# Kernel optimization log

Measured on AMD Instinct MI355X. Metric: run time of the kernel, lower is better.

The kernel has to match this reference:

```python
import jax, jax.numpy as jnp
import numpy as np

H = 64; DS = 32; DT = 24; ED = 16; OUT = 2
N = 10000       # nodes per type
E = 40000       # edges per edge type (before self loops)
MAX_DEG = 12    # static padded neighbor-sequence length (PyG to_dense_batch max); excess dropped


def setup_inputs() -> dict:
    key = jax.random.key(0)
    k = iter(jax.random.split(key, 40))
    def lin(o, i):
        s = 1.0 / np.sqrt(i)
        return jax.random.uniform(next(k), (o, i), jnp.float32, -s, s)
    inp = {}
    inp["x_source"] = jax.random.normal(next(k), (N, DS), jnp.float32)
    inp["x_target"] = jax.random.normal(next(k), (N, DT), jnp.float32)
    # 4 edge types in order [src->src, tgt->tgt, src->tgt, tgt->src], each [2, E]
    inp["edges"] = jax.random.randint(next(k), (4, 2, E), 0, N, dtype=jnp.int32)
    inp["edge_attr_st"] = jax.random.normal(next(k), (E, ED), jnp.float32)
    # node encoders (Linear-ReLU-Dropout(eval)-Linear)
    inp["We_s1"] = lin(H, DS); inp["be_s1"] = jnp.zeros((H,), jnp.float32)
    inp["We_s2"] = lin(H, H);  inp["be_s2"] = jnp.zeros((H,), jnp.float32)
    inp["We_t1"] = lin(H, DT); inp["be_t1"] = jnp.zeros((H,), jnp.float32)
    inp["We_t2"] = lin(H, H);  inp["be_t2"] = jnp.zeros((H,), jnp.float32)
    # 12 SAGEConv(aggr='lstm') blocks: 3 layers x 4 edge types, stacked on dim 0
    s = 1.0 / np.sqrt(H)
    inp["Wih"] = jax.random.uniform(next(k), (12, 4 * H, H), jnp.float32, -s, s)
    inp["Whh"] = jax.random.uniform(next(k), (12, 4 * H, H), jnp.float32, -s, s)
    inp["bih"] = jax.random.uniform(next(k), (12, 4 * H), jnp.float32, -s, s)
    inp["bhh"] = jax.random.uniform(next(k), (12, 4 * H), jnp.float32, -s, s)
    inp["Wl"]  = jax.random.uniform(next(k), (12, H, H), jnp.float32, -s, s)
    inp["bl"]  = jnp.zeros((12, H), jnp.float32)
    inp["Wr"]  = jax.random.uniform(next(k), (12, H, H), jnp.float32, -s, s)
    # edge gate + edge MLP head
    inp["Wg1"] = lin(H, 2 * H);   inp["bg1"] = jnp.zeros((H,), jnp.float32)
    inp["Wg2"] = lin(1, H);       inp["bg2"] = jnp.zeros((1,), jnp.float32)
    inp["Wm1"] = lin(H, H + ED);  inp["bm1"] = jnp.zeros((H,), jnp.float32)
    inp["Wm2"] = lin(H // 2, H);  inp["bm2"] = jnp.zeros((H // 2,), jnp.float32)
    inp["Wm3"] = lin(OUT, H // 2); inp["bm3"] = jnp.zeros((OUT,), jnp.float32)
    return inp


def _lstm_last(dense, Wih, Whh, bih, bhh):
    # dense: [n, T, H] padded neighbor sequences; PyG LSTMAggregation returns lstm(x)[0][:, -1]
    n = dense.shape[0]
    h0 = jnp.zeros((n, H), dense.dtype)
    def step(carry, x_t):
        h, c = carry
        g = x_t @ Wih.T + bih + h @ Whh.T + bhh  # torch gate order: i, f, g, o
        i, f, gg, o = jnp.split(g, 4, axis=-1)
        c = jax.nn.sigmoid(f) * c + jax.nn.sigmoid(i) * jnp.tanh(gg)
        h = jax.nn.sigmoid(o) * jnp.tanh(c)
        return (h, c), None
    (h, _), _ = jax.lax.scan(step, (h0, h0), jnp.swapaxes(dense, 0, 1))
    return h


def _sage_lstm(x_src, x_dst, src, dst, Wih, Whh, bih, bhh, Wl, bl, Wr):
    n_src, n_dst = x_src.shape[0], x_dst.shape[0]
    # add_self_loops(num_nodes=n_dst): appends (i, i) for every destination node, zero edge_attr
    loop = jnp.arange(n_dst, dtype=src.dtype)
    src = jnp.concatenate([src, loop]); dst = jnp.concatenate([dst, loop])
    # sort_edge_index(sort_by_row=False): stable lexicographic (dst, src) order
    order = jnp.argsort(dst.astype(jnp.int64) * n_src + src.astype(jnp.int64))
    src_s, dst_s = src[order], dst[order]
    xj = x_src[src_s]                                   # gather neighbor feats [E', H]
    deg = jnp.zeros((n_dst,), jnp.int32).at[dst_s].add(1)
    start = jnp.cumsum(deg) - deg                       # CSR row starts
    pos = jnp.arange(dst_s.shape[0], dtype=jnp.int32) - start[dst_s]
    dense = jnp.zeros((n_dst, MAX_DEG, x_src.shape[1]), x_src.dtype)
    dense = dense.at[dst_s, pos].set(xj, mode="drop")   # pad-to-dense, drop beyond MAX_DEG
    agg = _lstm_last(dense, Wih, Whh, bih, bhh)
    # SAGEConv: lin_l(aggr) + lin_r(x_root); lin_r has no bias
    return agg @ Wl.T + bl + x_dst @ Wr.T


def reference(x_source, x_target, edges, edge_attr_st,
              We_s1, be_s1, We_s2, be_s2, We_t1, be_t1, We_t2, be_t2,
              Wih, Whh, bih, bhh, Wl, bl, Wr,
              Wg1, bg1, Wg2, bg2, Wm1, bm1, Wm2, bm2, Wm3, bm3):
    relu = jax.nn.relu
    xs = relu(x_source @ We_s1.T + be_s1) @ We_s2.T + be_s2
    xt = relu(x_target @ We_t1.T + be_t1) @ We_t2.T + be_t2

    def layer(xs, xt, L):
        specs = [(xs, xs, 0), (xt, xt, 1), (xs, xt, 2), (xt, xs, 3)]
        outs = []
        for x_src, x_dst, et in specs:
            i = L * 4 + et
            outs.append(_sage_lstm(x_src, x_dst, edges[et, 0], edges[et, 1],
                                   Wih[i], Whh[i], bih[i], bhh[i], Wl[i], bl[i], Wr[i]))
        # HeteroConv(aggr='mean'): each node type receives from exactly 2 edge types
        return 0.5 * (outs[0] + outs[3]), 0.5 * (outs[1] + outs[2])

    s1, t1 = layer(xs, xt, 0); s1, t1 = relu(s1), relu(t1)
    s2, t2 = layer(s1, t1, 1); s2, t2 = relu(s2 + s1), relu(t2 + t1)
    s3, t3 = layer(s2, t2, 2); s3, t3 = relu(s3 + s2), relu(t3 + t2)

    # edge head on the main ('source','to','target') edges (original edges, no self loops)
    se, te = s3[edges[2, 0]], t3[edges[2, 1]]
    g = jax.nn.sigmoid(relu(jnp.concatenate([se, te], -1) @ Wg1.T + bg1) @ Wg2.T + bg2)
    er = g * se + (1.0 - g) * te
    h = relu(jnp.concatenate([er, edge_attr_st], -1) @ Wm1.T + bm1)
    h = relu(h @ Wm2.T + bm2)
    return h @ Wm3.T + bm3  # [E, OUT] edge logits
```

## Files before the change

### kernel.cpp

```cpp
#include <hip/hip_runtime.h>

#define N_NODES 10000
#define N_EDGES 40000
#define HD 64
#define MAXD 12
#define CAP 32
#define YROW ((size_t)(N_NODES + 1) * 256)

typedef __attribute__((ext_vector_type(8))) short short8;
typedef __attribute__((ext_vector_type(4))) float floatx4;

#define MFMA16(A, B, C) __builtin_amdgcn_mfma_f32_16x16x32_bf16(A, B, C, 0, 0, 0)

__device__ __forceinline__ float sigmoidf_(float x) {
  return 1.0f / (1.0f + __expf(-x));
}
__device__ __forceinline__ float fma4(float4 w, float4 x, float a) {
  a = fmaf(w.x, x.x, a);
  a = fmaf(w.y, x.y, a);
  a = fmaf(w.z, x.z, a);
  return fmaf(w.w, x.w, a);
}

__device__ __forceinline__ void split_frag(float4 a, float4 b, short8& hi, short8& lo) {
  float f[8] = {a.x, a.y, a.z, a.w, b.x, b.y, b.z, b.w};
  union { short8 v; unsigned d[4]; } H, L;
#pragma unroll
  for (int p = 0; p < 4; ++p) {
    unsigned u0 = __float_as_uint(f[2 * p]);
    unsigned u1 = __float_as_uint(f[2 * p + 1]);
    H.d[p] = (u0 >> 16) | (u1 & 0xFFFF0000u);
    float l0 = f[2 * p] - __uint_as_float(u0 & 0xFFFF0000u);
    float l1 = f[2 * p + 1] - __uint_as_float(u1 & 0xFFFF0000u);
    L.d[p] = (__float_as_uint(l0) >> 16) | (__float_as_uint(l1) & 0xFFFF0000u);
  }
  hi = H.v;
  lo = L.v;
}


__global__ void scatter_kernel(const int* __restrict__ edges, int* __restrict__ cnt,
                               int* __restrict__ pool) {
  int idx = blockIdx.x * 256 + threadIdx.x;
  if (idx >= 4 * N_EDGES) return;
  int et = idx / N_EDGES, e = idx - et * N_EDGES;
  int src = edges[(et * 2) * N_EDGES + e];
  int dst = edges[(et * 2 + 1) * N_EDGES + e];
  int slot = atomicAdd(&cnt[et * N_NODES + dst], 1);
  if (slot < CAP) pool[(et * N_NODES + dst) * CAP + slot] = src;
}

__global__ void sortrows_kernel(const int* __restrict__ cnt, const int* __restrict__ pool,
                                int* __restrict__ nbr) {
  __shared__ int buf[64][CAP + 1];
  int idx = blockIdx.x * 64 + threadIdx.x;
  if (idx >= 4 * N_NODES) return;
  int n = idx % N_NODES;
  int c = cnt[idx];
  if (c > CAP) c = CAP;
  int* a = buf[threadIdx.x];
  const int* row = pool + idx * CAP;
  for (int j = 0; j < c; ++j) a[j] = row[j] * 2;
  a[c] = n * 2 + 1;
  ++c;
  for (int i2 = 1; i2 < c; ++i2) {
    int key = a[i2];
    int b = i2 - 1;
    while (b >= 0 && a[b] > key) { a[b + 1] = a[b]; --b; }
    a[b + 1] = key;
  }
  int* onbr = nbr + idx * MAXD;
  for (int t = 0; t < MAXD; ++t) onbr[t] = (t < c) ? (a[t] >> 1) : N_NODES;
}

__global__ void zero_dummy_kernel(float* __restrict__ ybase) {
  int tid = threadIdx.x;
#pragma unroll
  for (int et = 0; et < 4; ++et)
    ybase[(size_t)et * YROW + (size_t)N_NODES * 256 + tid] = 0.0f;
}


__global__ __launch_bounds__(256) void prep_wfrag_kernel(const float* __restrict__ W,
                                                         short* __restrict__ w16) {
  int gid = blockIdx.x * 256 + threadIdx.x;
  if (gid >= 384 * 64) return;
  int lane = gid & 63;
  int combo = gid >> 6;
  int kc = combo & 1;
  int g = (combo >> 1) & 3;
  int w = (combo >> 3) & 3;
  int i = combo >> 5;
  int gate = g * 64 + w * 16 + (lane & 15);
  int k0 = kc * 32 + (lane >> 4) * 8;
  const float* src = W + ((size_t)i * 256 + gate) * 64 + k0;
  float4 a = ((const float4*)src)[0];
  float4 b = ((const float4*)src)[1];
  short8 hi, lo;
  split_frag(a, b, hi, lo);
  short8* dst = (short8*)w16;
  dst[(combo * 2 + 0) * 64 + lane] = hi;
  dst[(combo * 2 + 1) * 64 + lane] = lo;
}


__global__ __launch_bounds__(256) void prep_cw_kernel(const float* __restrict__ Wl,
    const float* __restrict__ Wr, short* __restrict__ cw) {
  int gid = blockIdx.x * 256 + threadIdx.x;
  if (gid >= 144 * 64) return;
  int lane = gid & 63;
  int rest = gid >> 6;
  int combo = rest & 7;
  int mat = (rest >> 3) % 3;
  int pair = rest / 24;
  int L = pair >> 1, side = pair & 1;
  int iA = L * 4 + (side ? 1 : 0);
  int iB = L * 4 + (side ? 2 : 3);
  int wp = combo >> 1, kc = combo & 1;
  int row = wp * 16 + (lane & 15);
  int k0 = kc * 32 + (lane >> 4) * 8;
  float4 a, b;
  if (mat == 0) {
    const float* s = Wl + ((size_t)iA * 64 + row) * 64 + k0;
    a = ((const float4*)s)[0]; b = ((const float4*)s)[1];
  } else if (mat == 1) {
    const float* s = Wl + ((size_t)iB * 64 + row) * 64 + k0;
    a = ((const float4*)s)[0]; b = ((const float4*)s)[1];
  } else {
    const float* sA = Wr + ((size_t)iA * 64 + row) * 64 + k0;
    const float* sB = Wr + ((size_t)iB * 64 + row) * 64 + k0;
    float4 a1 = ((const float4*)sA)[0], b1 = ((const float4*)sA)[1];
    float4 a2 = ((const float4*)sB)[0], b2 = ((const float4*)sB)[1];
    a.x = a1.x + a2.x; a.y = a1.y + a2.y; a.z = a1.z + a2.z; a.w = a1.w + a2.w;
    b.x = b1.x + b2.x; b.y = b1.y + b2.y; b.z = b1.z + b2.z; b.w = b1.w + b2.w;
  }
  short8 hi, lo;
  split_frag(a, b, hi, lo);
  short8* dst = (short8*)cw;
  int base = ((pair * 3 + mat) * 8 + combo) * 2;
  dst[(base + 0) * 64 + lane] = hi;
  dst[(base + 1) * 64 + lane] = lo;
}


template <int IN>
__global__ __launch_bounds__(256) void encode_kernel(const float* __restrict__ x,
    const float* __restrict__ W1, const float* __restrict__ b1,
    const float* __restrict__ W2, const float* __restrict__ b2, float* __restrict__ out) {
  __shared__ float xs[4][IN];
  __shared__ float h1[4][HD];
  int w = threadIdx.x >> 6, l = threadIdx.x & 63;
  int n = blockIdx.x * 4 + w;
  if (l < IN) xs[w][l] = x[n * IN + l];
  __syncthreads();
  float acc = b1[l];
#pragma unroll
  for (int k = 0; k < IN; ++k) acc = fmaf(xs[w][k], W1[l * IN + k], acc);
  h1[w][l] = fmaxf(acc, 0.0f);
  __syncthreads();
  float acc2 = b2[l];
#pragma unroll
  for (int k = 0; k < HD; ++k) acc2 = fmaf(h1[w][k], W2[l * HD + k], acc2);
  out[n * HD + l] = acc2;
}


__global__ __launch_bounds__(256) void ygemm_mfma_kernel(const float* __restrict__ xs0,
    const float* __restrict__ xt0, const short* __restrict__ wih16L, float* __restrict__ ybase) {
  __shared__ __align__(16) float xS[16][68];
  __shared__ __align__(16) float pS[16][260];
  int et = blockIdx.y;
  const float* x = (et == 0 || et == 2) ? xs0 : xt0;
  const short8* wf = (const short8*)(wih16L + (size_t)et * 32768);
  float* y = ybase + (size_t)et * YROW;
  int tid = threadIdx.x, w = tid >> 6, l = tid & 63;
  int quad = l >> 4, n = l & 15;
  int n0 = blockIdx.x * 16;
  {
    int node = tid >> 4, f4 = tid & 15;
    float4 v = *(const float4*)(x + (size_t)(n0 + node) * 64 + f4 * 4);
    *(float4*)&xS[node][f4 * 4] = v;
  }
  short8 Bh[4][2], Bl[4][2];
#pragma unroll
  for (int wp = 0; wp < 4; ++wp)
#pragma unroll
    for (int kc = 0; kc < 2; ++kc) {
      int combo = (wp * 4 + w) * 2 + kc;
      Bh[wp][kc] = wf[(combo * 2 + 0) * 64 + l];
      Bl[wp][kc] = wf[(combo * 2 + 1) * 64 + l];
    }
  __syncthreads();
  short8 Ah[2], Al[2];
  {
    const float* hp = &xS[n][quad * 8];
    float4 q0 = *(const float4*)hp, q1 = *(const float4*)(hp + 4);
    float4 q2 = *(const float4*)(hp + 32), q3 = *(const float4*)(hp + 36);
    split_frag(q0, q1, Ah[0], Al[0]);
    split_frag(q2, q3, Ah[1], Al[1]);
  }
  floatx4 acc[4];
#pragma unroll
  for (int wp = 0; wp < 4; ++wp) {
    floatx4 a = {0.f, 0.f, 0.f, 0.f};
    a = MFMA16(Ah[0], Bh[wp][0], a);
    a = MFMA16(Ah[1], Bh[wp][1], a);
    a = MFMA16(Al[0], Bh[wp][0], a);
    a = MFMA16(Al[1], Bh[wp][1], a);
    a = MFMA16(Ah[0], Bl[wp][0], a);
    a = MFMA16(Ah[1], Bl[wp][1], a);
    acc[wp] = a;
  }
#pragma unroll
  for (int wp = 0; wp < 4; ++wp)
#pragma unroll
    for (int r = 0; r < 4; ++r)
      pS[quad * 4 + r][(wp * 16 + n) * 4 + w] = acc[wp][r];
  __syncthreads();
#pragma unroll
  for (int cc = 0; cc < 4; ++cc) {
    int g4 = cc * 256 + tid;
    int node = g4 >> 6, col = g4 & 63;
    float4 v = *(const float4*)&pS[node][col * 4];
    ((float4*)(y + (size_t)(n0 + node) * 256))[col] = v;
  }
}


__global__ __launch_bounds__(256) void lstm_mfma_kernel(const int* __restrict__ nbrAll,
    const float* __restrict__ ybase, const short* __restrict__ whh16L,
    const float* __restrict__ bihL, const float* __restrict__ bhhL, float* __restrict__ aggBase) {
  __shared__ __align__(16) unsigned pkS[2][16 * 68];
  __shared__ int nbS[16][MAXD];
  int et = blockIdx.y;
  const int* nbr = nbrAll + (size_t)et * N_NODES * MAXD;
  const float4* y4 = (const float4*)(ybase + (size_t)et * YROW);
  const short* whh16 = whh16L + (size_t)et * 32768;
  const float* bih = bihL + et * 256;
  const float* bhh = bhhL + et * 256;
  float* agg = aggBase + (size_t)et * N_NODES * HD;
  int tid = threadIdx.x, w = tid >> 6, l = tid & 63;
  int quad = l >> 4, n = l & 15, u = w * 16 + n;
  int n0 = blockIdx.x * 16;
  if (tid < 16 * MAXD) ((int*)nbS)[tid] = nbr[n0 * MAXD + tid];
  short8 Bh[4][2], Bl[4][2];
  {
    const short8* wf = (const short8*)whh16;
#pragma unroll
    for (int g = 0; g < 4; ++g)
#pragma unroll
      for (int kc = 0; kc < 2; ++kc) {
        int combo = (w * 4 + g) * 2 + kc;
        Bh[g][kc] = wf[(combo * 2 + 0) * 64 + l];
        Bl[g][kc] = wf[(combo * 2 + 1) * 64 + l];
      }
  }
  float bs[4];
#pragma unroll
  for (int g = 0; g < 4; ++g) bs[g] = bih[g * 64 + u] + bhh[g * 64 + u];
  float c[4] = {0.f, 0.f, 0.f, 0.f}, h[4];
  short8 Ah[2], Al[2];
#pragma unroll
  for (int kc = 0; kc < 2; ++kc) { Ah[kc] = (short8)0; Al[kc] = (short8)0; }
  __syncthreads();
  float4 Y[4];
#pragma unroll
  for (int r = 0; r < 4; ++r) Y[r] = y4[(size_t)nbS[quad * 4 + r][0] * 64 + u];
  for (int t = 0; t < MAXD; ++t) {
    float yg[4][4];
#pragma unroll
    for (int r = 0; r < 4; ++r) {
      yg[0][r] = Y[r].x; yg[1][r] = Y[r].y; yg[2][r] = Y[r].z; yg[3][r] = Y[r].w;
    }
    floatx4 acc[4];
#pragma unroll
    for (int g = 0; g < 4; ++g) {
      floatx4 a = {yg[g][0], yg[g][1], yg[g][2], yg[g][3]};
      a = MFMA16(Ah[0], Bh[g][0], a);
      a = MFMA16(Ah[1], Bh[g][1], a);
      a = MFMA16(Al[0], Bh[g][0], a);
      a = MFMA16(Al[1], Bh[g][1], a);
      a = MFMA16(Ah[0], Bl[g][0], a);
      a = MFMA16(Ah[1], Bl[g][1], a);
      acc[g] = a;
    }
    if (t + 1 < MAXD) {
#pragma unroll
      for (int r = 0; r < 4; ++r) Y[r] = y4[(size_t)nbS[quad * 4 + r][t + 1] * 64 + u];
    }
    int buf = (t + 1) & 1;
#pragma unroll
    for (int r = 0; r < 4; ++r) {
      float gi = acc[0][r] + bs[0];
      float gf = acc[1][r] + bs[1];
      float gg = acc[2][r] + bs[2];
      float go = acc[3][r] + bs[3];
      float a_ = __expf(-gi);
      float b_ = __expf(fminf(-(gg + gg), 60.f));
      float f_ = __expf(-gf);
      float o_ = __expf(-go);
      float p1 = 1.f + a_, p2 = 1.f + b_, p3 = 1.f + f_;
      float d1 = p1 * p2;
      float num = fmaf(c[r], d1, (1.f - b_) * p3);
      c[r] = num * __builtin_amdgcn_rcpf(p3 * d1);
      float e_ = __expf(-(c[r] + c[r]));
      h[r] = (1.f - e_) * __builtin_amdgcn_rcpf((1.f + e_) * (1.f + o_));
      unsigned ub = __float_as_uint(h[r]);
      float lo = h[r] - __uint_as_float(ub & 0xFFFF0000u);
      pkS[buf][(quad * 4 + r) * 68 + u] =
          __builtin_amdgcn_perm(ub, __float_as_uint(lo), 0x07060302u);
    }
    __syncthreads();
    if (t + 1 < MAXD) {
#pragma unroll
      for (int kc = 0; kc < 2; ++kc) {
        const unsigned* pb = &pkS[buf][n * 68 + kc * 32 + quad * 8];
        uint4 qa = *(const uint4*)pb;
        uint4 qb = *(const uint4*)(pb + 4);
        union { short8 s; unsigned d[4]; } H, L;
        H.d[0] = __builtin_amdgcn_perm(qa.y, qa.x, 0x07060302u);
        H.d[1] = __builtin_amdgcn_perm(qa.w, qa.z, 0x07060302u);
        H.d[2] = __builtin_amdgcn_perm(qb.y, qb.x, 0x07060302u);
        H.d[3] = __builtin_amdgcn_perm(qb.w, qb.z, 0x07060302u);
        L.d[0] = __builtin_amdgcn_perm(qa.y, qa.x, 0x05040100u);
        L.d[1] = __builtin_amdgcn_perm(qa.w, qa.z, 0x05040100u);
        L.d[2] = __builtin_amdgcn_perm(qb.y, qb.x, 0x05040100u);
        L.d[3] = __builtin_amdgcn_perm(qb.w, qb.z, 0x05040100u);
        Ah[kc] = H.s;
        Al[kc] = L.s;
      }
    }
  }
#pragma unroll
  for (int r = 0; r < 4; ++r)
    agg[(size_t)(n0 + quad * 4 + r) * HD + u] = h[r];
}


__global__ __launch_bounds__(256) void combine_mfma_kernel(const float* __restrict__ aggBase,
    const short* __restrict__ cwL, const float* __restrict__ blL,
    const float* __restrict__ xS0, const float* __restrict__ xT0, int has_res,
    float* __restrict__ outS, float* __restrict__ outT) {
  __shared__ __align__(16) float tS[3][16][68];
  int side = blockIdx.y;
  int etA = side ? 1 : 0, etB = side ? 2 : 3;
  const float* srcs[3];
  srcs[0] = aggBase + (size_t)etA * N_NODES * HD;
  srcs[1] = aggBase + (size_t)etB * N_NODES * HD;
  srcs[2] = side ? xT0 : xS0;
  float* out = side ? outT : outS;
  const short8* wf = (const short8*)cwL + (size_t)side * 3072;
  const float* blA = blL + etA * 64;
  const float* blB = blL + etB * 64;
  int tid = threadIdx.x, w = tid >> 6, l = tid & 63;
  int quad = l >> 4, n = l & 15;
  int n0 = blockIdx.x * 16;
  {
    int node = tid >> 4, f4 = tid & 15;
#pragma unroll
    for (int m = 0; m < 3; ++m) {
      float4 v = *(const float4*)(srcs[m] + (size_t)(n0 + node) * 64 + f4 * 4);
      *(float4*)&tS[m][node][f4 * 4] = v;
    }
  }
  short8 Bh[3][2], Bl[3][2];
#pragma unroll
  for (int m = 0; m < 3; ++m)
#pragma unroll
    for (int kc = 0; kc < 2; ++kc) {
      int base = (m * 8 + w * 2 + kc) * 2;
      Bh[m][kc] = wf[(base + 0) * 64 + l];
      Bl[m][kc] = wf[(base + 1) * 64 + l];
    }
  float bsum = blA[w * 16 + n] + blB[w * 16 + n];
  __syncthreads();
  floatx4 a = {0.f, 0.f, 0.f, 0.f};
#pragma unroll
  for (int m = 0; m < 3; ++m) {
    short8 Ah[2], Al[2];
    const float* hp = &tS[m][n][quad * 8];
    float4 q0 = *(const float4*)hp, q1 = *(const float4*)(hp + 4);
    float4 q2 = *(const float4*)(hp + 32), q3 = *(const float4*)(hp + 36);
    split_frag(q0, q1, Ah[0], Al[0]);
    split_frag(q2, q3, Ah[1], Al[1]);
    a = MFMA16(Ah[0], Bh[m][0], a);
    a = MFMA16(Ah[1], Bh[m][1], a);
    a = MFMA16(Al[0], Bh[m][0], a);
    a = MFMA16(Al[1], Bh[m][1], a);
    a = MFMA16(Ah[0], Bl[m][0], a);
    a = MFMA16(Ah[1], Bl[m][1], a);
  }
#pragma unroll
  for (int r = 0; r < 4; ++r) {
    int node = quad * 4 + r;
    float v = 0.5f * (a[r] + bsum);
    if (has_res) v += tS[2][node][w * 16 + n];
    out[(size_t)(n0 + node) * 64 + w * 16 + n] = fmaxf(v, 0.f);
  }
}


__global__ __launch_bounds__(256) void edge_head_kernel(
    const int* __restrict__ esrc, const int* __restrict__ edst, const float* __restrict__ ea,
    const float* __restrict__ s3, const float* __restrict__ t3,
    const float* __restrict__ Wg1, const float* __restrict__ bg1,
    const float* __restrict__ Wg2, const float* __restrict__ bg2,
    const float* __restrict__ Wm1, const float* __restrict__ bm1,
    const float* __restrict__ Wm2, const float* __restrict__ bm2,
    const float* __restrict__ Wm3, const float* __restrict__ bm3,
    float* __restrict__ out) {
  __shared__ __align__(16) float4 xS[64][32];
  __shared__ __align__(16) float4 eaS[64][4];
  int tid = threadIdx.x, w = tid >> 6, l = tid & 63;
  int e0 = blockIdx.x * 64;
  for (int idx = tid; idx < 2048; idx += 256) {
    int e = idx >> 5, kk = idx & 31;
    float4 v;
    if (kk < 16) v = ((const float4*)(s3 + (size_t)esrc[e0 + e] * 64))[kk];
    else         v = ((const float4*)(t3 + (size_t)edst[e0 + e] * 64))[kk - 16];
    xS[e][kk] = v;
  }
  {
    int e = tid >> 2, kk = tid & 3;
    eaS[e][kk] = ((const float4*)(ea + (size_t)(e0 + e) * 16))[kk];
  }
  __syncthreads();
  {
    float4 wr[32];
    const float4* W4 = (const float4*)(Wg1 + l * 128);
#pragma unroll
    for (int kk = 0; kk < 32; ++kk) wr[kk] = W4[kk];
    float bg = bg1[l], w2 = Wg2[l], b2 = bg2[0];
    for (int m0 = 0; m0 < 16; m0 += 4) {
      int e = w * 16 + m0;
      float a0 = bg, a1 = bg, a2 = bg, a3 = bg;
#pragma unroll
      for (int kk = 0; kk < 32; ++kk) {
        float4 wv = wr[kk];
        a0 = fma4(wv, xS[e + 0][kk], a0);
        a1 = fma4(wv, xS[e + 1][kk], a1);
        a2 = fma4(wv, xS[e + 2][kk], a2);
        a3 = fma4(wv, xS[e + 3][kk], a3);
      }
      a0 = fmaxf(a0, 0.f) * w2; a1 = fmaxf(a1, 0.f) * w2;
      a2 = fmaxf(a2, 0.f) * w2; a3 = fmaxf(a3, 0.f) * w2;
#pragma unroll
      for (int off = 32; off; off >>= 1) {
        a0 += __shfl_xor(a0, off); a1 += __shfl_xor(a1, off);
        a2 += __shfl_xor(a2, off); a3 += __shfl_xor(a3, off);
      }
      float g0 = sigmoidf_(a0 + b2), g1 = sigmoidf_(a1 + b2);
      float g2 = sigmoidf_(a2 + b2), g3 = sigmoidf_(a3 + b2);
      float* r0 = (float*)xS[e + 0]; float* r1 = (float*)xS[e + 1];
      float* r2 = (float*)xS[e + 2]; float* r3 = (float*)xS[e + 3];
      r0[l] = fmaf(g0, r0[l] - r0[64 + l], r0[64 + l]);
      r1[l] = fmaf(g1, r1[l] - r1[64 + l], r1[64 + l]);
      r2[l] = fmaf(g2, r2[l] - r2[64 + l], r2[64 + l]);
      r3[l] = fmaf(g3, r3[l] - r3[64 + l], r3[64 + l]);
    }
  }
  __syncthreads();
  {
    float4 wr[20];
    const float4* W4 = (const float4*)(Wm1 + l * 80);
#pragma unroll
    for (int kk = 0; kk < 20; ++kk) wr[kk] = W4[kk];
    float bm = bm1[l];
    float h2v[16];
    for (int m0 = 0; m0 < 16; m0 += 4) {
      int e = w * 16 + m0;
      float a0 = bm, a1 = bm, a2 = bm, a3 = bm;
#pragma unroll
      for (int kk = 0; kk < 16; ++kk) {
        float4 wv = wr[kk];
        a0 = fma4(wv, xS[e + 0][kk], a0);
        a1 = fma4(wv, xS[e + 1][kk], a1);
        a2 = fma4(wv, xS[e + 2][kk], a2);
        a3 = fma4(wv, xS[e + 3][kk], a3);
      }
#pragma unroll
      for (int kk = 0; kk < 4; ++kk) {
        float4 wv = wr[16 + kk];
        a0 = fma4(wv, eaS[e + 0][kk], a0);
        a1 = fma4(wv, eaS[e + 1][kk], a1);
        a2 = fma4(wv, eaS[e + 2][kk], a2);
        a3 = fma4(wv, eaS[e + 3][kk], a3);
      }
      h2v[m0 + 0] = fmaxf(a0, 0.f); h2v[m0 + 1] = fmaxf(a1, 0.f);
      h2v[m0 + 2] = fmaxf(a2, 0.f); h2v[m0 + 3] = fmaxf(a3, 0.f);
    }
#pragma unroll
    for (int m = 0; m < 16; ++m) ((float*)xS[w * 16 + m])[64 + l] = h2v[m];
  }
  __syncthreads();
  {
    int half = l >> 5, j = l & 31;
    float4 wr[16];
    const float4* W4 = (const float4*)(Wm2 + j * 64);
#pragma unroll
    for (int kk = 0; kk < 16; ++kk) wr[kk] = W4[kk];
    float bm = bm2[j], w3a = Wm3[j], w3b = Wm3[32 + j];
    float b3a = bm3[0], b3b = bm3[1];
    for (int mg = 0; mg < 16; mg += 2) {
      int m = mg + half, e = w * 16 + m;
      float acc = bm;
#pragma unroll
      for (int kk = 0; kk < 16; ++kk) acc = fma4(wr[kk], xS[e][16 + kk], acc);
      float h3 = fmaxf(acc, 0.f);
      float p0 = h3 * w3a, p1 = h3 * w3b;
#pragma unroll
      for (int off = 16; off; off >>= 1) {
        p0 += __shfl_xor(p0, off);
        p1 += __shfl_xor(p1, off);
      }
      if (j == 0) {
        int ge = e0 + e;
        out[ge * 2 + 0] = p0 + b3a;
        out[ge * 2 + 1] = p1 + b3b;
      }
    }
  }
}


extern "C" void kernel_launch(void* const* d_in, const int* in_sizes, int n_in, void* d_out,
                              int out_size, void* d_ws, size_t ws_size, hipStream_t stream) {
  const float* x_source = (const float*)d_in[0];
  const float* x_target = (const float*)d_in[1];
  const int* edges = (const int*)d_in[2];
  const float* edge_attr = (const float*)d_in[3];
  const float* We_s1 = (const float*)d_in[4];
  const float* be_s1 = (const float*)d_in[5];
  const float* We_s2 = (const float*)d_in[6];
  const float* be_s2 = (const float*)d_in[7];
  const float* We_t1 = (const float*)d_in[8];
  const float* be_t1 = (const float*)d_in[9];
  const float* We_t2 = (const float*)d_in[10];
  const float* be_t2 = (const float*)d_in[11];
  const float* Wih = (const float*)d_in[12];
  const float* Whh = (const float*)d_in[13];
  const float* bih = (const float*)d_in[14];
  const float* bhh = (const float*)d_in[15];
  const float* Wl = (const float*)d_in[16];
  const float* bl = (const float*)d_in[17];
  const float* Wr = (const float*)d_in[18];
  const float* Wg1 = (const float*)d_in[19];
  const float* bg1 = (const float*)d_in[20];
  const float* Wg2 = (const float*)d_in[21];
  const float* bg2 = (const float*)d_in[22];
  const float* Wm1 = (const float*)d_in[23];
  const float* bm1 = (const float*)d_in[24];
  const float* Wm2 = (const float*)d_in[25];
  const float* bm2 = (const float*)d_in[26];
  const float* Wm3 = (const float*)d_in[27];
  const float* bm3 = (const float*)d_in[28];
  float* out = (float*)d_out;

  int* nbr = (int*)d_ws;
  int* cnt = nbr + 4 * N_NODES * MAXD;
  int* pool = cnt + 4 * N_NODES;
  float* fb = (float*)(pool + 4 * N_NODES * CAP);
  float* bufS[2] = {fb, fb + N_NODES * HD};
  float* bufT[2] = {fb + 2 * N_NODES * HD, fb + 3 * N_NODES * HD};
  float* aggBase = fb + (size_t)4 * N_NODES * HD;
  float* y4 = fb + (size_t)8 * N_NODES * HD;
  short* whh16 = (short*)(y4 + 4 * YROW);
  short* wih16 = whh16 + 12 * 32768;
  short* cw16 = wih16 + 12 * 32768;

  hipMemsetAsync(cnt, 0, 4 * N_NODES * sizeof(int), stream);
  prep_wfrag_kernel<<<96, 256, 0, stream>>>(Whh, whh16);
  prep_wfrag_kernel<<<96, 256, 0, stream>>>(Wih, wih16);
  prep_cw_kernel<<<36, 256, 0, stream>>>(Wl, Wr, cw16);
  zero_dummy_kernel<<<1, 256, 0, stream>>>(y4);
  scatter_kernel<<<(4 * N_EDGES + 255) / 256, 256, 0, stream>>>(edges, cnt, pool);
  sortrows_kernel<<<(4 * N_NODES + 63) / 64, 64, 0, stream>>>(cnt, pool, nbr);
  encode_kernel<32><<<N_NODES / 4, 256, 0, stream>>>(x_source, We_s1, be_s1, We_s2, be_s2, bufS[0]);
  encode_kernel<24><<<N_NODES / 4, 256, 0, stream>>>(x_target, We_t1, be_t1, We_t2, be_t2, bufT[0]);

  int cur = 0;
  for (int L = 0; L < 3; ++L) {
    ygemm_mfma_kernel<<<dim3(N_NODES / 16, 4), 256, 0, stream>>>(bufS[cur], bufT[cur],
        wih16 + (size_t)L * 4 * 32768, y4);
    lstm_mfma_kernel<<<dim3(N_NODES / 16, 4), 256, 0, stream>>>(nbr, y4,
        whh16 + (size_t)L * 4 * 32768, bih + L * 1024, bhh + L * 1024, aggBase);
    combine_mfma_kernel<<<dim3(N_NODES / 16, 2), 256, 0, stream>>>(aggBase,
        cw16 + (size_t)L * 2 * 24576, bl + L * 256,
        bufS[cur], bufT[cur], L > 0 ? 1 : 0, bufS[1 - cur], bufT[1 - cur]);
    cur = 1 - cur;
  }

  edge_head_kernel<<<N_EDGES / 64, 256, 0, stream>>>(edges + 4 * N_EDGES, edges + 5 * N_EDGES,
      edge_attr, bufS[cur], bufT[cur], Wg1, bg1, Wg2, bg2, Wm1, bm1, Wm2, bm2, Wm3, bm3, out);
}
```

Baseline: 489.4 us.

## Port edge head to split-bf16 MFMA, fuse prep/encode launches, fold log2e into LSTM weights

Replaces the scalar-FMA edge head with an MFMA version that uses hi/lo bf16 split weights prepared once in a fused prep kernel. The prep kernels, the dummy-row zeroing and the two encoder launches are merged into fewer launches. The LSTM weights and biases are pre-scaled by log2(e) so gate activations can use native exp2. Together these aim to cut FP32 ALU time in the edge head, launch overhead and transcendental cost, at some risk of small numerical differences from the split-bf16 products that omit the lo*lo term.

```diff
diff --git a/kernel.cpp b/kernel.cpp
--- a/kernel.cpp
+++ b/kernel.cpp
@@ -6,11 +6,19 @@
 #define MAXD 12
 #define CAP 32
 #define YROW ((size_t)(N_NODES + 1) * 256)
+#define LOG2E 1.44269504f
+#define XST 148
 
 typedef __attribute__((ext_vector_type(8))) short short8;
 typedef __attribute__((ext_vector_type(4))) float floatx4;
 
 #define MFMA16(A, B, C) __builtin_amdgcn_mfma_f32_16x16x32_bf16(A, B, C, 0, 0, 0)
+
+#if __has_builtin(__builtin_amdgcn_exp2f)
+#define EXP2(x) __builtin_amdgcn_exp2f(x)
+#else
+#define EXP2(x) __expf((x) * 0.6931471806f)
+#endif
 
 __device__ __forceinline__ float sigmoidf_(float x) {
   return 1.0f / (1.0f + __expf(-x));
@@ -73,29 +81,23 @@
   for (int t = 0; t < MAXD; ++t) onbr[t] = (t < c) ? (a[t] >> 1) : N_NODES;
 }
 
-__global__ void zero_dummy_kernel(float* __restrict__ ybase) {
-  int tid = threadIdx.x;
-#pragma unroll
-  for (int et = 0; et < 4; ++et)
-    ybase[(size_t)et * YROW + (size_t)N_NODES * 256 + tid] = 0.0f;
-}
-
-
-__global__ __launch_bounds__(256) void prep_wfrag_kernel(const float* __restrict__ W,
-                                                         short* __restrict__ w16) {
-  int gid = blockIdx.x * 256 + threadIdx.x;
-  if (gid >= 384 * 64) return;
+
+__device__ __forceinline__ void wfrag_body(const float* __restrict__ W,
+                                           short* __restrict__ w16, int gid) {
   int lane = gid & 63;
   int combo = gid >> 6;
   int kc = combo & 1;
   int g = (combo >> 1) & 3;
   int w = (combo >> 3) & 3;
   int i = combo >> 5;
+  float sc = (g == 2) ? (2.0f * LOG2E) : LOG2E;
   int gate = g * 64 + w * 16 + (lane & 15);
   int k0 = kc * 32 + (lane >> 4) * 8;
   const float* src = W + ((size_t)i * 256 + gate) * 64 + k0;
   float4 a = ((const float4*)src)[0];
   float4 b = ((const float4*)src)[1];
+  a.x *= sc; a.y *= sc; a.z *= sc; a.w *= sc;
+  b.x *= sc; b.y *= sc; b.z *= sc; b.w *= sc;
   short8 hi, lo;
   split_frag(a, b, hi, lo);
   short8* dst = (short8*)w16;
@@ -103,11 +105,8 @@
   dst[(combo * 2 + 1) * 64 + lane] = lo;
 }
 
-
-__global__ __launch_bounds__(256) void prep_cw_kernel(const float* __restrict__ Wl,
-    const float* __restrict__ Wr, short* __restrict__ cw) {
-  int gid = blockIdx.x * 256 + threadIdx.x;
-  if (gid >= 144 * 64) return;
+__device__ __forceinline__ void cw_body(const float* __restrict__ Wl,
+    const float* __restrict__ Wr, short* __restrict__ cw, int gid) {
   int lane = gid & 63;
   int rest = gid >> 6;
   int combo = rest & 7;
@@ -142,9 +141,64 @@
   dst[(base + 1) * 64 + lane] = lo;
 }
 
+__device__ __forceinline__ void eh_body(const float* __restrict__ Wg1,
+    const float* __restrict__ Wm1, const float* __restrict__ Wm2,
+    short* __restrict__ ehw16, int gid) {
+  int lane = gid & 63;
+  int combo = gid >> 6;
+  int n = lane & 15, quad = lane >> 4;
+  int mat, wp, kc;
+  if (combo < 16) { mat = 0; wp = combo >> 2; kc = combo & 3; }
+  else if (combo < 28) { int c2 = combo - 16; mat = 1; wp = c2 / 3; kc = c2 % 3; }
+  else { int c2 = combo - 28; mat = 2; wp = c2 >> 1; kc = c2 & 1; }
+  int row = wp * 16 + n;
+  int k0 = kc * 32 + quad * 8;
+  float4 a = {0.f, 0.f, 0.f, 0.f}, b = {0.f, 0.f, 0.f, 0.f};
+  if (mat == 0) {
+    const float* s = Wg1 + (size_t)row * 128 + k0;
+    a = ((const float4*)s)[0]; b = ((const float4*)s)[1];
+  } else if (mat == 1) {
+    if (k0 + 8 <= 80) {
+      const float* s = Wm1 + (size_t)row * 80 + k0;
+      a = ((const float4*)s)[0]; b = ((const float4*)s)[1];
+    }
+  } else {
+    const float* s = Wm2 + (size_t)row * 64 + k0;
+    a = ((const float4*)s)[0]; b = ((const float4*)s)[1];
+  }
+  short8 hi, lo;
+  split_frag(a, b, hi, lo);
+  short8* dst = (short8*)ehw16;
+  dst[(combo * 2 + 0) * 64 + lane] = hi;
+  dst[(combo * 2 + 1) * 64 + lane] = lo;
+}
+
+__global__ __launch_bounds__(256) void prep_all_kernel(
+    const float* __restrict__ Whh, const float* __restrict__ Wih,
+    const float* __restrict__ Wl, const float* __restrict__ Wr,
+    const float* __restrict__ Wg1, const float* __restrict__ Wm1,
+    const float* __restrict__ Wm2,
+    short* __restrict__ whh16, short* __restrict__ wih16, short* __restrict__ cw16,
+    short* __restrict__ ehw16, float* __restrict__ ybase) {
+  int gid = blockIdx.x * 256 + threadIdx.x;
+  if (gid < 24576) {
+    wfrag_body(Whh, whh16, gid);
+  } else if (gid < 49152) {
+    wfrag_body(Wih, wih16, gid - 24576);
+  } else if (gid < 58368) {
+    cw_body(Wl, Wr, cw16, gid - 49152);
+  } else if (gid < 60416) {
+    eh_body(Wg1, Wm1, Wm2, ehw16, gid - 58368);
+  } else if (gid < 61440) {
+    int t = gid - 60416;
+    int et = t >> 8, col = t & 255;
+    ybase[(size_t)et * YROW + (size_t)N_NODES * 256 + col] = 0.0f;
+  }
+}
+
 
 template <int IN>
-__global__ __launch_bounds__(256) void encode_kernel(const float* __restrict__ x,
+__device__ __forceinline__ void encode_body(const float* __restrict__ x,
     const float* __restrict__ W1, const float* __restrict__ b1,
     const float* __restrict__ W2, const float* __restrict__ b2, float* __restrict__ out) {
   __shared__ float xs[4][IN];
@@ -162,6 +216,17 @@
 #pragma unroll
   for (int k = 0; k < HD; ++k) acc2 = fmaf(h1[w][k], W2[l * HD + k], acc2);
   out[n * HD + l] = acc2;
+}
+
+__global__ __launch_bounds__(256) void encode_both_kernel(
+    const float* __restrict__ xs0, const float* __restrict__ xt0,
+    const float* __restrict__ Ws1, const float* __restrict__ bs1,
+    const float* __restrict__ Ws2, const float* __restrict__ bs2,
+    const float* __restrict__ Wt1, const float* __restrict__ bt1,
+    const float* __restrict__ Wt2, const float* __restrict__ bt2,
+    float* __restrict__ outS, float* __restrict__ outT) {
+  if (blockIdx.y == 0) encode_body<32>(xs0, Ws1, bs1, Ws2, bs2, outS);
+  else encode_body<24>(xt0, Wt1, bt1, Wt2, bt2, outT);
 }
 
 
@@ -257,7 +322,8 @@
   }
   float bs[4];
 #pragma unroll
-  for (int g = 0; g < 4; ++g) bs[g] = bih[g * 64 + u] + bhh[g * 64 + u];
+  for (int g = 0; g < 4; ++g)
+    bs[g] = (bih[g * 64 + u] + bhh[g * 64 + u]) * ((g == 2) ? (2.0f * LOG2E) : LOG2E);
   float c[4] = {0.f, 0.f, 0.f, 0.f}, h[4];
   short8 Ah[2], Al[2];
 #pragma unroll
@@ -295,15 +361,15 @@
       float gf = acc[1][r] + bs[1];
       float gg = acc[2][r] + bs[2];
       float go = acc[3][r] + bs[3];
-      float a_ = __expf(-gi);
-      float b_ = __expf(fminf(-(gg + gg), 60.f));
-      float f_ = __expf(-gf);
-      float o_ = __expf(-go);
+      float a_ = EXP2(-gi);
+      float b_ = EXP2(fminf(-gg, 60.f));
+      float f_ = EXP2(-gf);
+      float o_ = EXP2(-go);
       float p1 = 1.f + a_, p2 = 1.f + b_, p3 = 1.f + f_;
       float d1 = p1 * p2;
       float num = fmaf(c[r], d1, (1.f - b_) * p3);
       c[r] = num * __builtin_amdgcn_rcpf(p3 * d1);
-      float e_ = __expf(-(c[r] + c[r]));
+      float e_ = EXP2(c[r] * (-2.0f * LOG2E));
       h[r] = (1.f - e_) * __builtin_amdgcn_rcpf((1.f + e_) * (1.f + o_));
       unsigned ub = __float_as_uint(h[r]);
       float lo = h[r] - __uint_as_float(ub & 0xFFFF0000u);
@@ -400,125 +466,177 @@
 }
 
 
-__global__ __launch_bounds__(256) void edge_head_kernel(
+__global__ __launch_bounds__(256) void edge_head_mfma_kernel(
     const int* __restrict__ esrc, const int* __restrict__ edst, const float* __restrict__ ea,
     const float* __restrict__ s3, const float* __restrict__ t3,
-    const float* __restrict__ Wg1, const float* __restrict__ bg1,
-    const float* __restrict__ Wg2, const float* __restrict__ bg2,
-    const float* __restrict__ Wm1, const float* __restrict__ bm1,
-    const float* __restrict__ Wm2, const float* __restrict__ bm2,
-    const float* __restrict__ Wm3, const float* __restrict__ bm3,
-    float* __restrict__ out) {
-  __shared__ __align__(16) float4 xS[64][32];
-  __shared__ __align__(16) float4 eaS[64][4];
+    const short* __restrict__ ehw16,
+    const float* __restrict__ bg1, const float* __restrict__ Wg2,
+    const float* __restrict__ bg2, const float* __restrict__ bm1,
+    const float* __restrict__ bm2, const float* __restrict__ Wm3,
+    const float* __restrict__ bm3, float* __restrict__ out) {
+  __shared__ __align__(16) float xS[64][XST];
+  __shared__ float gP[4][64];
   int tid = threadIdx.x, w = tid >> 6, l = tid & 63;
+  int quad = l >> 4, n = l & 15;
   int e0 = blockIdx.x * 64;
+  const short8* wf = (const short8*)ehw16;
   for (int idx = tid; idx < 2048; idx += 256) {
     int e = idx >> 5, kk = idx & 31;
     float4 v;
     if (kk < 16) v = ((const float4*)(s3 + (size_t)esrc[e0 + e] * 64))[kk];
     else         v = ((const float4*)(t3 + (size_t)edst[e0 + e] * 64))[kk - 16];
-    xS[e][kk] = v;
+    *(float4*)&xS[e][kk * 4] = v;
   }
   {
     int e = tid >> 2, kk = tid & 3;
-    eaS[e][kk] = ((const float4*)(ea + (size_t)(e0 + e) * 16))[kk];
-  }
-  __syncthreads();
-  {
-    float4 wr[32];
-    const float4* W4 = (const float4*)(Wg1 + l * 128);
-#pragma unroll
-    for (int kk = 0; kk < 32; ++kk) wr[kk] = W4[kk];
-    float bg = bg1[l], w2 = Wg2[l], b2 = bg2[0];
-    for (int m0 = 0; m0 < 16; m0 += 4) {
-      int e = w * 16 + m0;
-      float a0 = bg, a1 = bg, a2 = bg, a3 = bg;
-#pragma unroll
-      for (int kk = 0; kk < 32; ++kk) {
-        float4 wv = wr[kk];
-        a0 = fma4(wv, xS[e + 0][kk], a0);
-        a1 = fma4(wv, xS[e + 1][kk], a1);
-        a2 = fma4(wv, xS[e + 2][kk], a2);
-        a3 = fma4(wv, xS[e + 3][kk], a3);
+    *(float4*)&xS[e][128 + kk * 4] = ((const float4*)(ea + (size_t)(e0 + e) * 16))[kk];
+  }
+  __syncthreads();
+  {
+    short8 Bh[4], Bl[4];
+#pragma unroll
+    for (int kc = 0; kc < 4; ++kc) {
+      int cb = w * 4 + kc;
+      Bh[kc] = wf[(cb * 2 + 0) * 64 + l];
+      Bl[kc] = wf[(cb * 2 + 1) * 64 + l];
+    }
+    float bg = bg1[w * 16 + n];
+    float wg2l = Wg2[w * 16 + n];
+    float red[4][4];
+#pragma unroll
+    for (int mt = 0; mt < 4; ++mt) {
+      floatx4 a = {bg, bg, bg, bg};
+#pragma unroll
+      for (int kc = 0; kc < 4; ++kc) {
+        const float* hp = &xS[mt * 16 + n][kc * 32 + quad * 8];
+        float4 q0 = *(const float4*)hp, q1 = *(const float4*)(hp + 4);
+        short8 Ah, Al;
+        split_frag(q0, q1, Ah, Al);
+        a = MFMA16(Ah, Bh[kc], a);
+        a = MFMA16(Al, Bh[kc], a);
+        a = MFMA16(Ah, Bl[kc], a);
       }
-      a0 = fmaxf(a0, 0.f) * w2; a1 = fmaxf(a1, 0.f) * w2;
-      a2 = fmaxf(a2, 0.f) * w2; a3 = fmaxf(a3, 0.f) * w2;
-#pragma unroll
-      for (int off = 32; off; off >>= 1) {
-        a0 += __shfl_xor(a0, off); a1 += __shfl_xor(a1, off);
-        a2 += __shfl_xor(a2, off); a3 += __shfl_xor(a3, off);
+#pragma unroll
+      for (int r = 0; r < 4; ++r) red[mt][r] = fmaxf(a[r], 0.f) * wg2l;
+    }
+#pragma unroll
+    for (int mt = 0; mt < 4; ++mt)
+#pragma unroll
+      for (int r = 0; r < 4; ++r) {
+#pragma unroll
+        for (int off = 1; off < 16; off <<= 1)
+          red[mt][r] += __shfl_xor(red[mt][r], off);
       }
-      float g0 = sigmoidf_(a0 + b2), g1 = sigmoidf_(a1 + b2);
-      float g2 = sigmoidf_(a2 + b2), g3 = sigmoidf_(a3 + b2);
-      float* r0 = (float*)xS[e + 0]; float* r1 = (float*)xS[e + 1];
-      float* r2 = (float*)xS[e + 2]; float* r3 = (float*)xS[e + 3];
-      r0[l] = fmaf(g0, r0[l] - r0[64 + l], r0[64 + l]);
-      r1[l] = fmaf(g1, r1[l] - r1[64 + l], r1[64 + l]);
-      r2[l] = fmaf(g2, r2[l] - r2[64 + l], r2[64 + l]);
-      r3[l] = fmaf(g3, r3[l] - r3[64 + l], r3[64 + l]);
-    }
-  }
-  __syncthreads();
-  {
-    float4 wr[20];
-    const float4* W4 = (const float4*)(Wm1 + l * 80);
-#pragma unroll
-    for (int kk = 0; kk < 20; ++kk) wr[kk] = W4[kk];
-    float bm = bm1[l];
-    float h2v[16];
-    for (int m0 = 0; m0 < 16; m0 += 4) {
-      int e = w * 16 + m0;
-      float a0 = bm, a1 = bm, a2 = bm, a3 = bm;
-#pragma unroll
-      for (int kk = 0; kk < 16; ++kk) {
-        float4 wv = wr[kk];
-        a0 = fma4(wv, xS[e + 0][kk], a0);
-        a1 = fma4(wv, xS[e + 1][kk], a1);
-        a2 = fma4(wv, xS[e + 2][kk], a2);
-        a3 = fma4(wv, xS[e + 3][kk], a3);
+#pragma unroll
+    for (int mt = 0; mt < 4; ++mt)
+#pragma unroll
+      for (int r = 0; r < 4; ++r)
+        if (n == mt * 4 + r) gP[w][mt * 16 + quad * 4 + r] = red[mt][r];
+  }
+  __syncthreads();
+  float gv[4];
+  {
+    float b2 = bg2[0];
+#pragma unroll
+    for (int mt = 0; mt < 4; ++mt) {
+      int e = mt * 16 + n;
+      float p = gP[0][e] + gP[1][e] + gP[2][e] + gP[3][e] + b2;
+      gv[mt] = sigmoidf_(p);
+    }
+  }
+  floatx4 acc2[4];
+  {
+    short8 Bh[3], Bl[3];
+#pragma unroll
+    for (int kc = 0; kc < 3; ++kc) {
+      int cb = 16 + w * 3 + kc;
+      Bh[kc] = wf[(cb * 2 + 0) * 64 + l];
+      Bl[kc] = wf[(cb * 2 + 1) * 64 + l];
+    }
+    float bm = bm1[w * 16 + n];
+#pragma unroll
+    for (int mt = 0; mt < 4; ++mt) {
+      int e = mt * 16 + n;
+      float g = gv[mt];
+      floatx4 a = {bm, bm, bm, bm};
+#pragma unroll
+      for (int kc = 0; kc < 2; ++kc) {
+        const float* sp = &xS[e][kc * 32 + quad * 8];
+        float4 s0 = *(const float4*)sp, s1 = *(const float4*)(sp + 4);
+        float4 t0 = *(const float4*)(sp + 64), t1 = *(const float4*)(sp + 68);
+        float4 e0v, e1v;
+        e0v.x = fmaf(g, s0.x - t0.x, t0.x); e0v.y = fmaf(g, s0.y - t0.y, t0.y);
+        e0v.z = fmaf(g, s0.z - t0.z, t0.z); e0v.w = fmaf(g, s0.w - t0.w, t0.w);
+        e1v.x = fmaf(g, s1.x - t1.x, t1.x); e1v.y = fmaf(g, s1.y - t1.y, t1.y);
+        e1v.z = fmaf(g, s1.z - t1.z, t1.z); e1v.w = fmaf(g, s1.w - t1.w, t1.w);
+        short8 Ah, Al;
+        split_frag(e0v, e1v, Ah, Al);
+        a = MFMA16(Ah, Bh[kc], a);
+        a = MFMA16(Al, Bh[kc], a);
+        a = MFMA16(Ah, Bl[kc], a);
       }
-#pragma unroll
-      for (int kk = 0; kk < 4; ++kk) {
-        float4 wv = wr[16 + kk];
-        a0 = fma4(wv, eaS[e + 0][kk], a0);
-        a1 = fma4(wv, eaS[e + 1][kk], a1);
-        a2 = fma4(wv, eaS[e + 2][kk], a2);
-        a3 = fma4(wv, eaS[e + 3][kk], a3);
+      {
+        float4 z0 = {0.f, 0.f, 0.f, 0.f}, z1 = {0.f, 0.f, 0.f, 0.f};
+        if (quad < 2) {
+          const float* ap = &xS[e][128 + quad * 8];
+          z0 = *(const float4*)ap;
+          z1 = *(const float4*)(ap + 4);
+        }
+        short8 Ah, Al;
+        split_frag(z0, z1, Ah, Al);
+        a = MFMA16(Ah, Bh[2], a);
+        a = MFMA16(Al, Bh[2], a);
+        a = MFMA16(Ah, Bl[2], a);
       }
-      h2v[m0 + 0] = fmaxf(a0, 0.f); h2v[m0 + 1] = fmaxf(a1, 0.f);
-      h2v[m0 + 2] = fmaxf(a2, 0.f); h2v[m0 + 3] = fmaxf(a3, 0.f);
-    }
-#pragma unroll
-    for (int m = 0; m < 16; ++m) ((float*)xS[w * 16 + m])[64 + l] = h2v[m];
-  }
-  __syncthreads();
-  {
-    int half = l >> 5, j = l & 31;
-    float4 wr[16];
-    const float4* W4 = (const float4*)(Wm2 + j * 64);
-#pragma unroll
-    for (int kk = 0; kk < 16; ++kk) wr[kk] = W4[kk];
-    float bm = bm2[j], w3a = Wm3[j], w3b = Wm3[32 + j];
-    float b3a = bm3[0], b3b = bm3[1];
-    for (int mg = 0; mg < 16; mg += 2) {
-      int m = mg + half, e = w * 16 + m;
-      float acc = bm;
-#pragma unroll
-      for (int kk = 0; kk < 16; ++kk) acc = fma4(wr[kk], xS[e][16 + kk], acc);
-      float h3 = fmaxf(acc, 0.f);
-      float p0 = h3 * w3a, p1 = h3 * w3b;
-#pragma unroll
-      for (int off = 16; off; off >>= 1) {
-        p0 += __shfl_xor(p0, off);
-        p1 += __shfl_xor(p1, off);
+      acc2[mt] = a;
+    }
+  }
+  __syncthreads();
+#pragma unroll
+  for (int mt = 0; mt < 4; ++mt)
+#pragma unroll
+    for (int r = 0; r < 4; ++r)
+      xS[mt * 16 + quad * 4 + r][w * 16 + n] = fmaxf(acc2[mt][r], 0.f);
+  __syncthreads();
+  {
+    int s = w & 1, mtb = (w >> 1) * 2;
+    short8 Bh[2], Bl[2];
+#pragma unroll
+    for (int kc = 0; kc < 2; ++kc) {
+      int cb = 28 + s * 2 + kc;
+      Bh[kc] = wf[(cb * 2 + 0) * 64 + l];
+      Bl[kc] = wf[(cb * 2 + 1) * 64 + l];
+    }
+    float bm = bm2[s * 16 + n];
+#pragma unroll
+    for (int mi = 0; mi < 2; ++mi) {
+      int mt = mtb + mi;
+      int e = mt * 16 + n;
+      floatx4 a = {bm, bm, bm, bm};
+#pragma unroll
+      for (int kc = 0; kc < 2; ++kc) {
+        const float* sp = &xS[e][kc * 32 + quad * 8];
+        float4 q0 = *(const float4*)sp, q1 = *(const float4*)(sp + 4);
+        short8 Ah, Al;
+        split_frag(q0, q1, Ah, Al);
+        a = MFMA16(Ah, Bh[kc], a);
+        a = MFMA16(Al, Bh[kc], a);
+        a = MFMA16(Ah, Bl[kc], a);
       }
-      if (j == 0) {
-        int ge = e0 + e;
-        out[ge * 2 + 0] = p0 + b3a;
-        out[ge * 2 + 1] = p1 + b3b;
-      }
-    }
+#pragma unroll
+      for (int r = 0; r < 4; ++r)
+        xS[mt * 16 + quad * 4 + r][64 + s * 16 + n] = fmaxf(a[r], 0.f);
+    }
+  }
+  __syncthreads();
+  if (tid < 128) {
+    int e = tid >> 1, j = tid & 1;
+    const float4* hp = (const float4*)&xS[e][64];
+    const float4* w3 = (const float4*)(Wm3 + j * 32);
+    float a = bm3[j];
+#pragma unroll
+    for (int kk = 0; kk < 8; ++kk) a = fma4(w3[kk], hp[kk], a);
+    out[(e0 + e) * 2 + j] = a;
   }
 }
 
@@ -567,16 +685,15 @@
   short* whh16 = (short*)(y4 + 4 * YROW);
   short* wih16 = whh16 + 12 * 32768;
   short* cw16 = wih16 + 12 * 32768;
+  short* ehw16 = cw16 + 6 * 24576;
 
   hipMemsetAsync(cnt, 0, 4 * N_NODES * sizeof(int), stream);
-  prep_wfrag_kernel<<<96, 256, 0, stream>>>(Whh, whh16);
-  prep_wfrag_kernel<<<96, 256, 0, stream>>>(Wih, wih16);
-  prep_cw_kernel<<<36, 256, 0, stream>>>(Wl, Wr, cw16);
-  zero_dummy_kernel<<<1, 256, 0, stream>>>(y4);
+  prep_all_kernel<<<240, 256, 0, stream>>>(Whh, Wih, Wl, Wr, Wg1, Wm1, Wm2,
+      whh16, wih16, cw16, ehw16, y4);
   scatter_kernel<<<(4 * N_EDGES + 255) / 256, 256, 0, stream>>>(edges, cnt, pool);
   sortrows_kernel<<<(4 * N_NODES + 63) / 64, 64, 0, stream>>>(cnt, pool, nbr);
-  encode_kernel<32><<<N_NODES / 4, 256, 0, stream>>>(x_source, We_s1, be_s1, We_s2, be_s2, bufS[0]);
-  encode_kernel<24><<<N_NODES / 4, 256, 0, stream>>>(x_target, We_t1, be_t1, We_t2, be_t2, bufT[0]);
+  encode_both_kernel<<<dim3(N_NODES / 4, 2), 256, 0, stream>>>(x_source, x_target,
+      We_s1, be_s1, We_s2, be_s2, We_t1, be_t1, We_t2, be_t2, bufS[0], bufT[0]);
 
   int cur = 0;
   for (int L = 0; L < 3; ++L) {
@@ -590,6 +707,7 @@
     cur = 1 - cur;
   }
 
-  edge_head_kernel<<<N_EDGES / 64, 256, 0, stream>>>(edges + 4 * N_EDGES, edges + 5 * N_EDGES,
-      edge_attr, bufS[cur], bufT[cur], Wg1, bg1, Wg2, bg2, Wm1, bm1, Wm2, bm2, Wm3, bm3, out);
-}
+  edge_head_mfma_kernel<<<N_EDGES / 64, 256, 0, stream>>>(edges + 4 * N_EDGES,
+      edges + 5 * N_EDGES, edge_attr, bufS[cur], bufT[cur], ehw16,
+      bg1, Wg2, bg2, bm1, bm2, Wm3, bm3, out);
+}
```

Result: faster. 444.4 us (-9.2%).
